# Optimization experiments

Measured on AMD Instinct MI355X. Metric: run time of the kernel, lower is better.

Reference implementation:

```python
import jax, jax.numpy as jnp
import numpy as np

N_EMBD = 1024
N_HEAD = 16
HEAD_DIM = N_EMBD // N_HEAD


def setup_inputs() -> dict:
    key = jax.random.key(0)
    kx, kq, kk, kv, ko = jax.random.split(key, 5)
    B, T = 4, 2048
    std = 1.0 / np.sqrt(N_EMBD)
    return {
        "x": jax.random.normal(kx, (B, T, N_EMBD), dtype=jnp.float32),
        "wq": jax.random.normal(kq, (N_EMBD, N_EMBD), dtype=jnp.float32) * std,
        "wk": jax.random.normal(kk, (N_EMBD, N_EMBD), dtype=jnp.float32) * std,
        "wv": jax.random.normal(kv, (N_EMBD, N_EMBD), dtype=jnp.float32) * std,
        "wo": jax.random.normal(ko, (N_EMBD, N_EMBD), dtype=jnp.float32) * std,
    }


def reference(x, wq, wk, wv, wo):
    B, T, C = x.shape
    # nn.Linear(x) = x @ W.T; weights stored as (out, in)
    def proj(w):
        return jnp.einsum('btc,dc->btd', x, w).reshape(B, T, N_HEAD, HEAD_DIM).transpose(0, 2, 1, 3)
    q, k, v = proj(wq), proj(wk), proj(wv)  # [B,H,T,Dh]
    scale = HEAD_DIM ** -0.5
    attn = jnp.einsum('bhtd,bhsd->bhts', q, k) * scale  # [B,H,T,T]
    causal = jnp.tril(jnp.ones((T, T), dtype=bool))
    attn = jnp.where(causal, attn, -jnp.inf)
    attn = jax.nn.softmax(attn, axis=-1)
    out = jnp.einsum('bhts,bhsd->bhtd', attn, v)  # [B,H,T,Dh]
    out = out.transpose(0, 2, 1, 3).reshape(B, T, C)
    return jnp.einsum('btc,dc->btd', out, wo)
```

## Files before the change

kernel.cpp:

```cpp
#include <hip/hip_runtime.h>
#include <hip/hip_bf16.h>
#include <stdint.h>

typedef __attribute__((ext_vector_type(8))) __bf16 bf16x8;
typedef __attribute__((ext_vector_type(4))) __bf16 bf16x4;
typedef __attribute__((ext_vector_type(4))) float  f32x4;

#define MFMA16(a, b, c) __builtin_amdgcn_mfma_f32_16x16x32_bf16((a), (b), (c), 0, 0, 0)

#define GLD16(gp, lp) __builtin_amdgcn_global_load_lds(                                   \
    (const __attribute__((address_space(1))) uint32_t*)(gp),                              \
    (__attribute__((address_space(3))) uint32_t*)(lp), 16, 0, 0)

#define BB 4
#define TT 2048
#define CC 1024
#define HH 16
#define DH 64
#define GM 8192
#define GN 1024
#define GK 1024

__global__ __launch_bounds__(256) void cvt_all_kernel(const float* __restrict__ x,
                                                      const float* __restrict__ w0,
                                                      const float* __restrict__ w1,
                                                      const float* __restrict__ w2,
                                                      const float* __restrict__ w3,
                                                      __bf16* __restrict__ xb,
                                                      __bf16* __restrict__ wb) {
    int gb = blockIdx.x;
    const float* src;
    __bf16* dst;
    int i;
    if (gb < 4096) {
        src = x; dst = xb;
        i = gb * 256 + threadIdx.x;
    } else {
        int g = gb - 4096;
        int wz = g >> 9, lb = g & 511;
        const float* srcs[4] = {w0, w1, w2, w3};
        src = srcs[wz]; dst = wb + (size_t)wz * CC * CC;
        i = lb * 256 + threadIdx.x;
    }
    const float4* s = (const float4*)src + (size_t)i * 2;
    float4 f0 = s[0], f1 = s[1];
    bf16x8 h;
    h[0] = (__bf16)f0.x; h[1] = (__bf16)f0.y; h[2] = (__bf16)f0.z; h[3] = (__bf16)f0.w;
    h[4] = (__bf16)f1.x; h[5] = (__bf16)f1.y; h[6] = (__bf16)f1.z; h[7] = (__bf16)f1.w;
    *(bf16x8*)(dst + (size_t)i * 8) = h;
}

__global__ __launch_bounds__(256) void transpose_kernel(const __bf16* __restrict__ V,
                                                        __bf16* __restrict__ VT) {
    __shared__ __bf16 Ts[64][72];
    int tid = threadIdx.x;
    int m0 = blockIdx.x * 64, c0 = blockIdx.y * 64;
#pragma unroll
    for (int r = 0; r < 2; r++) {
        int ch = r * 256 + tid;
        int mm = ch >> 3, c8 = (ch & 7) * 8;
        *(uint4*)&Ts[mm][c8] = *(const uint4*)(V + (size_t)(m0 + mm) * CC + c0 + c8);
    }
    __syncthreads();
#pragma unroll
    for (int r = 0; r < 2; r++) {
        int ch = r * 256 + tid;
        int cc = ch >> 3, m8 = (ch & 7) * 8;
        bf16x8 v;
#pragma unroll
        for (int e = 0; e < 8; e++) v[e] = Ts[m8 + e][cc];
        *(bf16x8*)(VT + (size_t)(c0 + cc) * GM + m0 + m8) = v;
    }
}

__global__ __launch_bounds__(512, 2) void gemm8(const __bf16* __restrict__ A,
                                                const __bf16* __restrict__ Bmat,
                                                __bf16* __restrict__ Cbf,
                                                float* __restrict__ Cf) {
    __shared__ __align__(16) char lds[98304];
    char* ldsA = lds;
    char* ldsB = lds + 65536;

    int id = blockIdx.x;
    int xcd = id & 7, slot = id >> 3;
    int mb = xcd * 4 + (slot & 3);
    int nb = slot >> 2;
    int m0 = mb * 256, n0 = nb * 128;

    int tid  = threadIdx.x;
    int lane = tid & 63, w = tid >> 6;
    int wm = w >> 1, wn = w & 1;
    int l15 = lane & 15, q8 = lane >> 4;
    int x7  = l15 & 7;

    int arow = tid >> 3;
    int lc   = (tid & 7) ^ (arow & 7);
    const __bf16* Abase = A    + (size_t)(m0 + arow) * GK + lc * 8;
    const __bf16* Bbase = Bmat + (size_t)(n0 + arow) * GK + lc * 8;
    int wbase = (tid & ~63) * 16;

    int cb0 = ((q8)     ^ x7) * 16;
    int cb1 = ((q8 + 4) ^ x7) * 16;
    int arb0 = (wm * 32 + l15) * 128;
    int arb1 = (wm * 32 + 16 + l15) * 128;
    int brb0 = (wn * 32 + l15) * 128;
    int brb1 = (wn * 32 + 16 + l15) * 128;

    f32x4 zero = {0.f, 0.f, 0.f, 0.f};
    f32x4 acc[4][4];
#pragma unroll
    for (int i = 0; i < 4; i++)
#pragma unroll
        for (int j = 0; j < 4; j++) acc[i][j] = zero;

    bf16x8 areg[2][2];
    bf16x8 breg[4][2];

#define STAGE_A(T_, H_) do {                                                              \
        const __bf16* _g = Abase + (size_t)((H_) * 128) * GK + (((T_) & 15) * 64);        \
        char* _d = ldsA + ((((T_) & 1) * 2 + (H_)) * 16384) + wbase;                      \
        GLD16(_g, _d);                                                                    \
        GLD16(_g + (size_t)64 * GK, _d + 8192);                                           \
    } while (0)
#define STAGE_B(T_, H_) do {                                                              \
        const __bf16* _g = Bbase + (size_t)((H_) * 64) * GK + (((T_) & 15) * 64);         \
        GLD16(_g, ldsB + ((((T_) & 1) * 2 + (H_)) * 8192) + wbase);                       \
    } while (0)
#define LD_A(BK_, H_) do {                                                                \
        char* _p = ldsA + (((BK_) * 2 + (H_)) * 16384);                                   \
        areg[0][0] = *(const bf16x8*)(_p + arb0 + cb0);                                   \
        areg[0][1] = *(const bf16x8*)(_p + arb0 + cb1);                                   \
        areg[1][0] = *(const bf16x8*)(_p + arb1 + cb0);                                   \
        areg[1][1] = *(const bf16x8*)(_p + arb1 + cb1);                                   \
    } while (0)
#define LD_B(BK_, H_) do {                                                                \
        char* _p = ldsB + (((BK_) * 2 + (H_)) * 8192);                                    \
        breg[(H_) * 2 + 0][0] = *(const bf16x8*)(_p + brb0 + cb0);                        \
        breg[(H_) * 2 + 0][1] = *(const bf16x8*)(_p + brb0 + cb1);                        \
        breg[(H_) * 2 + 1][0] = *(const bf16x8*)(_p + brb1 + cb0);                        \
        breg[(H_) * 2 + 1][1] = *(const bf16x8*)(_p + brb1 + cb1);                        \
    } while (0)
#define QMFMA(MH_, N0_, N1_) do {                                                         \
        acc[(MH_)*2+0][N0_] = MFMA16(areg[0][0], breg[N0_][0], acc[(MH_)*2+0][N0_]);      \
        acc[(MH_)*2+0][N1_] = MFMA16(areg[0][0], breg[N1_][0], acc[(MH_)*2+0][N1_]);      \
        acc[(MH_)*2+1][N0_] = MFMA16(areg[1][0], breg[N0_][0], acc[(MH_)*2+1][N0_]);      \
        acc[(MH_)*2+1][N1_] = MFMA16(areg[1][0], breg[N1_][0], acc[(MH_)*2+1][N1_]);      \
        acc[(MH_)*2+0][N0_] = MFMA16(areg[0][1], breg[N0_][1], acc[(MH_)*2+0][N0_]);      \
        acc[(MH_)*2+0][N1_] = MFMA16(areg[0][1], breg[N1_][1], acc[(MH_)*2+0][N1_]);      \
        acc[(MH_)*2+1][N0_] = MFMA16(areg[1][1], breg[N0_][1], acc[(MH_)*2+1][N0_]);      \
        acc[(MH_)*2+1][N1_] = MFMA16(areg[1][1], breg[N1_][1], acc[(MH_)*2+1][N1_]);      \
    } while (0)
#define BAR   __builtin_amdgcn_s_barrier()
#define PRIO1 __builtin_amdgcn_s_setprio(1)
#define PRIO0 __builtin_amdgcn_s_setprio(0)
#define VM5   asm volatile("s_waitcnt vmcnt(5)" ::: "memory")

    STAGE_A(0, 0); STAGE_A(0, 1); STAGE_B(0, 0); STAGE_B(0, 1);
    STAGE_A(1, 0); STAGE_B(1, 1); STAGE_A(1, 1);
    VM5;
    BAR;

    for (int i = 0; i < 8; i++) {
        int t = 2 * i;
        LD_A(0, 0); LD_B(0, 0);
        STAGE_B(t + 1, 0);
        BAR; PRIO1; QMFMA(0, 0, 1); PRIO0; BAR;
        LD_B(0, 1);
        STAGE_A(t + 2, 0);
        BAR; PRIO1; QMFMA(0, 2, 3); PRIO0; BAR;
        LD_A(0, 1);
        STAGE_B(t + 2, 1);
        BAR; PRIO1; QMFMA(1, 2, 3); PRIO0; BAR;
        STAGE_A(t + 2, 1);
        BAR; PRIO1; QMFMA(1, 0, 1); PRIO0;
        VM5; BAR;
        LD_A(1, 0); LD_B(1, 0);
        STAGE_B(t + 2, 0);
        BAR; PRIO1; QMFMA(0, 0, 1); PRIO0; BAR;
        LD_B(1, 1);
        STAGE_A(t + 3, 0);
        BAR; PRIO1; QMFMA(0, 2, 3); PRIO0; BAR;
        LD_A(1, 1);
        STAGE_B(t + 3, 1);
        BAR; PRIO1; QMFMA(1, 2, 3); PRIO0; BAR;
        STAGE_A(t + 3, 1);
        BAR; PRIO1; QMFMA(1, 0, 1); PRIO0;
        VM5; BAR;
    }

    asm volatile("s_waitcnt vmcnt(0)" ::: "memory");

    int zc  = n0 >> 10;
    int ncb = n0 & 1023;
#pragma unroll
    for (int mt = 0; mt < 4; mt++) {
        int mrow = m0 + (mt >> 1) * 128 + wm * 32 + (mt & 1) * 16 + q8 * 4;
#pragma unroll
        for (int nt = 0; nt < 4; nt++) {
            int ncol = ncb + (nt >> 1) * 64 + wn * 32 + (nt & 1) * 16 + l15;
            f32x4 v = acc[mt][nt];
            if (Cf) {
                float* p = Cf + (size_t)mrow * GN + ncol;
                p[0] = v.x; p[GN] = v.y; p[2 * GN] = v.z; p[3 * GN] = v.w;
            } else {
                __bf16* p = Cbf + (size_t)zc * ((size_t)GM * GN) + (size_t)mrow * GN + ncol;
                p[0] = (__bf16)v.x; p[GN] = (__bf16)v.y;
                p[2 * GN] = (__bf16)v.z; p[3 * GN] = (__bf16)v.w;
            }
        }
    }
#undef STAGE_A
#undef STAGE_B
#undef LD_A
#undef LD_B
#undef QMFMA
#undef BAR
#undef PRIO1
#undef PRIO0
#undef VM5
}

__global__ __launch_bounds__(256) void attn_kernel(const __bf16* __restrict__ Q,
                                                   const __bf16* __restrict__ K,
                                                   const __bf16* __restrict__ VT,
                                                   __bf16* __restrict__ Y) {
    __shared__ __bf16 Ks[2][64 * 64];
    __shared__ __bf16 Vs[2][64 * 64];
    __shared__ __bf16 Ps[4][16 * 64];

    int tid  = threadIdx.x;
    int lane = tid & 63, w = tid >> 6;
    int l15 = lane & 15, q8 = lane >> 4;
    int y  = blockIdx.y, y0 = y & 3, kk = y >> 2;
    int qt = (kk & 1) ? (2 * y0 + (kk >> 1)) : (15 - (kk >> 1) - 2 * y0);
    int bh = blockIdx.x, b = bh >> 4, h = bh & 15;
    size_t rowb = (size_t)b * TT;
    const float SC = 0.125f * 1.44269504f;
    const float M2 = 12.0f * 1.44269504f;
    int ql = w * 16 + l15;
    int x7 = l15 & 7;

    bf16x8 qfr[2][2];
#pragma unroll
    for (int qf = 0; qf < 2; qf++) {
        int q = qt * 128 + qf * 64 + w * 16 + l15;
        const __bf16* qp = Q + (rowb + q) * CC + h * DH + q8 * 8;
        bf16x8 r0 = *(const bf16x8*)qp;
        bf16x8 r1 = *(const bf16x8*)(qp + 32);
#pragma unroll
        for (int e = 0; e < 8; e++) {
            r0[e] = (__bf16)((float)r0[e] * SC);
            r1[e] = (__bf16)((float)r1[e] * SC);
        }
        qfr[qf][0] = r0; qfr[qf][1] = r1;
    }

    f32x4 zero = {0.f, 0.f, 0.f, 0.f};
    f32x4 acc[2][5];
#pragma unroll
    for (int qf = 0; qf < 2; qf++)
#pragma unroll
        for (int t5 = 0; t5 < 5; t5++) acc[qf][t5] = zero;

    bf16x8 ones;
#pragma unroll
    for (int e = 0; e < 8; e++) ones[e] = (l15 == 0) ? (__bf16)1.0f : (__bf16)0.0f;

    int c0 = tid, c1 = tid + 256;
    int s0 = c0 >> 3, d80 = ((c0 & 7) ^ (s0 & 7)) * 8;
    int s1 = c1 >> 3, d81 = ((c1 & 7) ^ (s1 & 7)) * 8;
    const __bf16* Kg0 = K + (rowb + s0) * CC + h * DH + d80;
    const __bf16* Kg1 = K + (rowb + s1) * CC + h * DH + d81;
    const __bf16* Vg0 = VT + (size_t)(h * DH + s0) * GM + rowb + d80;
    const __bf16* Vg1 = VT + (size_t)(h * DH + s1) * GM + rowb + d81;
    char* KsB = (char*)Ks; char* VsB = (char*)Vs;
    int wbase = (tid & ~63) * 16;

    GLD16(Kg0, KsB + wbase);
    GLD16(Kg1, KsB + 4096 + wbase);
    GLD16(Vg0, VsB + wbase);
    GLD16(Vg1, VsB + 4096 + wbase);

    int jmax = 2 * qt + 1;
    for (int j = 0; j <= jmax; j++) {
        __syncthreads();
        if (j < jmax) {
            int bo = ((j + 1) & 1) * 8192;
            GLD16(Kg0 + (size_t)(j + 1) * 64 * CC, KsB + bo + wbase);
            GLD16(Kg1 + (size_t)(j + 1) * 64 * CC, KsB + bo + 4096 + wbase);
            GLD16(Vg0 + (j + 1) * 64, VsB + bo + wbase);
            GLD16(Vg1 + (j + 1) * 64, VsB + bo + 4096 + wbase);
        }
        const __bf16* Kc = &Ks[j & 1][0];
        const __bf16* Vc = &Vs[j & 1][0];
        bool do0 = (j != jmax);

        f32x4 s2[2][4];
#pragma unroll
        for (int st = 0; st < 4; st++) {
            bf16x8 k0f = *(const bf16x8*)(Kc + (st * 16 + l15) * 64 + ((q8 ^ x7) * 8));
            bf16x8 k1f = *(const bf16x8*)(Kc + (st * 16 + l15) * 64 + (((q8 + 4) ^ x7) * 8));
            f32x4 t1 = zero;
            t1 = MFMA16(k0f, qfr[1][0], t1);
            t1 = MFMA16(k1f, qfr[1][1], t1);
            s2[1][st] = t1;
            if (do0) {
                f32x4 t0 = zero;
                t0 = MFMA16(k0f, qfr[0][0], t0);
                t0 = MFMA16(k1f, qfr[0][1], t0);
                s2[0][st] = t0;
            }
        }

#pragma unroll
        for (int qf = 0; qf < 2; qf++) {
            if (qf == 0 && !do0) continue;
            if (j == 2 * qt + qf) {
#pragma unroll
                for (int st = 0; st < 4; st++) {
                    f32x4 t = s2[qf][st];
                    int sb = st * 16 + q8 * 4;
                    t.x = (sb + 0 > ql) ? -1e30f : t.x;
                    t.y = (sb + 1 > ql) ? -1e30f : t.y;
                    t.z = (sb + 2 > ql) ? -1e30f : t.z;
                    t.w = (sb + 3 > ql) ? -1e30f : t.w;
                    s2[qf][st] = t;
                }
            }
        }

        bf16x8 bp[2][2];
#pragma unroll
        for (int qf = 0; qf < 2; qf++) {
            if (qf == 0 && !do0) continue;
#pragma unroll
            for (int st = 0; st < 4; st++) {
                bf16x4 pk;
                pk[0] = (__bf16)__builtin_amdgcn_exp2f(s2[qf][st].x - M2);
                pk[1] = (__bf16)__builtin_amdgcn_exp2f(s2[qf][st].y - M2);
                pk[2] = (__bf16)__builtin_amdgcn_exp2f(s2[qf][st].z - M2);
                pk[3] = (__bf16)__builtin_amdgcn_exp2f(s2[qf][st].w - M2);
                int swzc = (st * 2 + (q8 >> 1)) ^ x7;
                *(bf16x4*)(Ps[w] + l15 * 64 + swzc * 8 + (q8 & 1) * 4) = pk;
            }
            bp[qf][0] = *(const bf16x8*)(Ps[w] + l15 * 64 + ((q8 ^ x7) * 8));
            bp[qf][1] = *(const bf16x8*)(Ps[w] + l15 * 64 + (((q8 + 4) ^ x7) * 8));
        }

#pragma unroll
        for (int dt = 0; dt < 4; dt++) {
            bf16x8 v0 = *(const bf16x8*)(Vc + (dt * 16 + l15) * 64 + ((q8 ^ x7) * 8));
            bf16x8 v1 = *(const bf16x8*)(Vc + (dt * 16 + l15) * 64 + (((q8 + 4) ^ x7) * 8));
            acc[1][dt] = MFMA16(v0, bp[1][0], acc[1][dt]);
            acc[1][dt] = MFMA16(v1, bp[1][1], acc[1][dt]);
            if (do0) {
                acc[0][dt] = MFMA16(v0, bp[0][0], acc[0][dt]);
                acc[0][dt] = MFMA16(v1, bp[0][1], acc[0][dt]);
            }
        }
        acc[1][4] = MFMA16(ones, bp[1][0], acc[1][4]);
        acc[1][4] = MFMA16(ones, bp[1][1], acc[1][4]);
        if (do0) {
            acc[0][4] = MFMA16(ones, bp[0][0], acc[0][4]);
            acc[0][4] = MFMA16(ones, bp[0][1], acc[0][4]);
        }
    }

#pragma unroll
    for (int qf = 0; qf < 2; qf++) {
        float lsum = __shfl(acc[qf][4].x, l15);
        float ri = 1.0f / lsum;
        int q = qt * 128 + qf * 64 + w * 16 + l15;
        __bf16* yp = Y + (rowb + q) * CC + h * DH + q8 * 4;
#pragma unroll
        for (int dt = 0; dt < 4; dt++) {
            bf16x4 o;
            o[0] = (__bf16)(acc[qf][dt].x * ri);
            o[1] = (__bf16)(acc[qf][dt].y * ri);
            o[2] = (__bf16)(acc[qf][dt].z * ri);
            o[3] = (__bf16)(acc[qf][dt].w * ri);
            *(bf16x4*)(yp + dt * 16) = o;
        }
    }
}

extern "C" void kernel_launch(void* const* d_in, const int* in_sizes, int n_in,
                              void* d_out, int out_size, void* d_ws, size_t ws_size,
                              hipStream_t stream) {
    const float* x  = (const float*)d_in[0];
    const float* wq = (const float*)d_in[1];
    const float* wk = (const float*)d_in[2];
    const float* wv = (const float*)d_in[3];
    const float* wo = (const float*)d_in[4];
    float* out = (float*)d_out;

    char* ws = (char*)d_ws;
    __bf16* xb  = (__bf16*)ws;
    __bf16* wb  = (__bf16*)(ws + (size_t)16777216);
    __bf16* qkv = (__bf16*)(ws + (size_t)25165824);
    __bf16* yb  = (__bf16*)(ws + (size_t)75497472);

    cvt_all_kernel<<<dim3(4096 + 4 * 512), 256, 0, stream>>>(x, wq, wk, wv, wo, xb, wb);
    gemm8<<<dim3(768), 512, 0, stream>>>(xb, wb, qkv, nullptr);
    transpose_kernel<<<dim3(GM / 64, GN / 64), 256, 0, stream>>>(
        qkv + (size_t)2 * GM * GN, xb);
    attn_kernel<<<dim3(BB * HH, 16), 256, 0, stream>>>(
        qkv, qkv + (size_t)GM * GN, xb, yb);
    gemm8<<<dim3(256), 512, 0, stream>>>(yb, wb + (size_t)3 * CC * CC, nullptr, out);
}
```

Before: 245.6 us.

## Restructure GEMM main loop into fewer, larger MFMA phases with retuned waits

Reorganizes the projection GEMM's software pipeline so each half-iteration runs two MFMA quads per barrier pair instead of one. This halves the number of barrier phases. Global-to-LDS staging is regrouped, and the vmcnt waits are retuned to 6 and 4 to match the new issue order. The aim is to cut barrier and synchronization overhead. In exchange, the prefetch distance for some stages gets shorter, which could expose load latency, and the waitcnt values must exactly match the staging order to stay correct.

```diff
diff --git a/kernel.cpp b/kernel.cpp
--- a/kernel.cpp
+++ b/kernel.cpp
@@ -153,39 +153,28 @@
 #define BAR   __builtin_amdgcn_s_barrier()
 #define PRIO1 __builtin_amdgcn_s_setprio(1)
 #define PRIO0 __builtin_amdgcn_s_setprio(0)
-#define VM5   asm volatile("s_waitcnt vmcnt(5)" ::: "memory")
-
-    STAGE_A(0, 0); STAGE_A(0, 1); STAGE_B(0, 0); STAGE_B(0, 1);
-    STAGE_A(1, 0); STAGE_B(1, 1); STAGE_A(1, 1);
-    VM5;
+#define VM6   asm volatile("s_waitcnt vmcnt(6)" ::: "memory")
+#define VM4   asm volatile("s_waitcnt vmcnt(4)" ::: "memory")
+
+    STAGE_B(0, 0); STAGE_B(0, 1); STAGE_A(0, 0); STAGE_A(0, 1);
+    STAGE_B(1, 0); STAGE_B(1, 1); STAGE_A(1, 0);
+    VM4;
     BAR;
 
     for (int i = 0; i < 8; i++) {
         int t = 2 * i;
-        LD_A(0, 0); LD_B(0, 0);
-        STAGE_B(t + 1, 0);
-        BAR; PRIO1; QMFMA(0, 0, 1); PRIO0; BAR;
-        LD_B(0, 1);
-        STAGE_A(t + 2, 0);
-        BAR; PRIO1; QMFMA(0, 2, 3); PRIO0; BAR;
+        LD_A(0, 0); LD_B(0, 0); LD_B(0, 1);
+        STAGE_A(t + 1, 1);
+        BAR; PRIO1; QMFMA(0, 0, 1); QMFMA(0, 2, 3); PRIO0; BAR;
         LD_A(0, 1);
-        STAGE_B(t + 2, 1);
-        BAR; PRIO1; QMFMA(1, 2, 3); PRIO0; BAR;
+        STAGE_B(t + 2, 0); STAGE_B(t + 2, 1); STAGE_A(t + 2, 0);
+        BAR; PRIO1; QMFMA(1, 0, 1); QMFMA(1, 2, 3); PRIO0; VM6; BAR;
+        LD_A(1, 0); LD_B(1, 0); LD_B(1, 1);
         STAGE_A(t + 2, 1);
-        BAR; PRIO1; QMFMA(1, 0, 1); PRIO0;
-        VM5; BAR;
-        LD_A(1, 0); LD_B(1, 0);
-        STAGE_B(t + 2, 0);
-        BAR; PRIO1; QMFMA(0, 0, 1); PRIO0; BAR;
-        LD_B(1, 1);
-        STAGE_A(t + 3, 0);
-        BAR; PRIO1; QMFMA(0, 2, 3); PRIO0; BAR;
+        BAR; PRIO1; QMFMA(0, 0, 1); QMFMA(0, 2, 3); PRIO0; VM6; BAR;
         LD_A(1, 1);
-        STAGE_B(t + 3, 1);
-        BAR; PRIO1; QMFMA(1, 2, 3); PRIO0; BAR;
-        STAGE_A(t + 3, 1);
-        BAR; PRIO1; QMFMA(1, 0, 1); PRIO0;
-        VM5; BAR;
+        STAGE_B(t + 3, 0); STAGE_B(t + 3, 1); STAGE_A(t + 3, 0);
+        BAR; PRIO1; QMFMA(1, 0, 1); QMFMA(1, 2, 3); PRIO0; VM4; BAR;
     }
 
     asm volatile("s_waitcnt vmcnt(0)" ::: "memory");
@@ -217,7 +206,8 @@
 #undef BAR
 #undef PRIO1
 #undef PRIO0
-#undef VM5
+#undef VM6
+#undef VM4
 }
 
 __global__ __launch_bounds__(256) void attn_kernel(const __bf16* __restrict__ Q,
```

Result: faster. 238.0 us (-3.1%).
